# Kernel tuning notes

Measured on AMD Instinct MI355X. Metric: run time of the kernel, lower is better.

Reference implementation:

```python
import jax, jax.numpy as jnp
import numpy as np

K = 16            # neighbors per node
NB = 8            # number_of_basis
MAX_RADIUS = 10.0
MUL_1E = 32       # multiplicity of the 1e output block
DIM_0E = 64       # 64x0e block (structurally zero: no 1o x 0e -> 0e path)
DIM_2E = 80       # 16x2e block (structurally zero: no 1o x 0e -> 2e path)


def knn_edges(coords):
    """coords [B,N,3] -> (senders, receivers) flat int32 indices of length B*N*K.
    Edge (j -> i): j is one of the K nearest neighbors of i (self excluded),
    matching torch_geometric knn_graph(loop=False, flow=source_to_target)."""
    B, N, _ = coords.shape
    n2 = jnp.sum(coords * coords, -1)                       # [B,N]
    d2 = n2[:, :, None] + n2[:, None, :] - 2.0 * jnp.einsum('bnd,bmd->bnm', coords, coords)
    d2 = d2 + jnp.eye(N, dtype=coords.dtype) * 1e10         # exclude self-loops
    _, idx = jax.lax.top_k(-d2, K)                          # [B,N,K] neighbor ids per node
    offs = (jnp.arange(B) * N)[:, None, None]
    senders = (idx + offs).reshape(-1)
    receivers = (jnp.broadcast_to(jnp.arange(N)[None, :, None], (B, N, K)) + offs).reshape(-1)
    return senders, receivers


def gaussian_soft_one_hot(x, number):
    # x in [0,1], shape [E,1] -> [E,number]
    centers = jnp.linspace(0.0, 1.0, number).astype(x.dtype)
    sigma = 1.0 / number
    g = jnp.exp(-(x - centers) ** 2 / (2.0 * sigma * sigma))
    s = jnp.sum(g, -1, keepdims=True)
    s = jnp.where(s > 0, s, jnp.ones_like(s))
    return g / s


def setup_inputs():
    key = jax.random.key(0)
    ks = jax.random.split(key, 6)
    B, N = 8, 4096
    coords = jax.random.normal(ks[0], (B, N, 3), dtype=jnp.float32) * 10.0
    atom_types = jax.random.randint(ks[1], (B, N), 0, 20)
    residue_types = jax.random.randint(ks[2], (B, N), 0, 21)
    tp_weight = jax.random.normal(ks[3], (NB, MUL_1E), dtype=jnp.float32) / np.sqrt(NB)
    atom_emb = jax.random.normal(ks[4], (20, 112), dtype=jnp.float32).at[0].set(0.0)   # padding_idx=0
    res_emb = jax.random.normal(ks[5], (21, 112), dtype=jnp.float32).at[0].set(0.0)    # padding_idx=0
    return {"coords": coords, "atom_types": atom_types, "residue_types": residue_types,
            "tp_weight": tp_weight, "atom_emb": atom_emb, "res_emb": res_emb}


def reference(coords, atom_types, residue_types, tp_weight, atom_emb, res_emb):
    B, N, _ = coords.shape
    E = B * N * K
    senders, receivers = knn_edges(coords)
    cf = coords.reshape(-1, 3)
    r = cf[senders] - cf[receivers]                           # [E,3]
    dist = jnp.linalg.norm(r, axis=-1, keepdims=True)         # [E,1]
    r_hat = r / (dist + 1e-8)
    cutoff = jnp.clip(dist / MAX_RADIUS, 0.0, 1.0)
    rb = gaussian_soft_one_hot(cutoff, NB)                    # [E,NB]
    # FullyConnectedTensorProduct(1x1o/1e, NBx0e -> ... 32x1e ...):
    feat_1e = jnp.einsum('ev,vw,em->ewm', rb, tp_weight, r_hat) / np.sqrt(3.0)  # [E,32,3]
    # scatter_mean over receivers
    num = jax.ops.segment_sum(feat_1e.reshape(E, MUL_1E * 3), receivers, num_segments=B * N)
    cnt = jax.ops.segment_sum(jnp.ones((E,), coords.dtype), receivers, num_segments=B * N)
    agg_1e = (num / jnp.maximum(cnt, 1.0)[:, None]).reshape(B, N, MUL_1E * 3)
    zeros0 = jnp.zeros((B, N, DIM_0E), coords.dtype)
    zeros2 = jnp.zeros((B, N, DIM_2E), coords.dtype)
    pos_feats = jnp.concatenate([zeros0, agg_1e, zeros2], -1)  # [B,N,240]
    node_features = jnp.concatenate([pos_feats, atom_emb[atom_types], res_emb[residue_types]], -1)
    return node_features  # [B,N,464]
```

## Files before the change

kernel.cpp:

```cpp
#include <hip/hip_runtime.h>
#include <hip/hip_bf16.h>

#define NN    4096
#define KNEI  16
#define QPW   4
#define WPB   16
#define BLOCK (WPB * 64)
#define QPB   (WPB * QPW)
#define BIGF  3.0e38f


__device__ __forceinline__ float wave_max_dpp(float v)
{
    float f = v;
#define STEPX(CTRL)                                                          \
    { int s_ = __builtin_amdgcn_update_dpp(__float_as_int(f),                \
               __float_as_int(f), (CTRL), 0xF, 0xF, false);                  \
      f = fmaxf(f, __int_as_float(s_)); }
    STEPX(0x111) STEPX(0x112) STEPX(0x114) STEPX(0x118) STEPX(0x142) STEPX(0x143)
#undef STEPX
    return f;
}

__device__ __forceinline__ int wave_min_i32_dpp(int v)
{
    int f = v;
#define STEPM(CTRL)                                                          \
    { int s_ = __builtin_amdgcn_update_dpp(f, f, (CTRL), 0xF, 0xF, false);   \
      f = min(f, s_); }
    STEPM(0x111) STEPM(0x112) STEPM(0x114) STEPM(0x118) STEPM(0x142) STEPM(0x143)
#undef STEPM
    return f;
}

__device__ __forceinline__ float row16_sum_dpp(float v)
{
    float f = v;
#define STEPA(CTRL)                                                          \
    { int s_ = __builtin_amdgcn_update_dpp(0, __float_as_int(f),             \
               (CTRL), 0xF, 0xF, true);                                      \
      f += __int_as_float(s_); }
    STEPA(0x111) STEPA(0x112) STEPA(0x114) STEPA(0x118)
#undef STEPA
    return f;
}

__device__ __forceinline__ float score_calc(const float4 P, float xi, float yi,
                                            float zi, int j, int iLoc)
{
    float s = fmaf(P.x, xi, fmaf(P.y, yi, fmaf(P.z, zi, P.w)));
    return (j == iLoc) ? -1.0e30f : s;
}

__device__ __forceinline__ void wave_argmax(float v, int idx,
                                            float& m, int& midx, int& w)
{
    float f = wave_max_dpp(v);
    float M = __int_as_float(__builtin_amdgcn_readlane(__float_as_int(f), 63));
    unsigned long long msk = __ballot(v == M);
    if (__popcll(msk) > 1) {
        int ci = (v == M) ? idx : 0x7fffffff;
        ci = wave_min_i32_dpp(ci);
        ci = __builtin_amdgcn_readlane(ci, 63);
        midx = ci;
        unsigned long long m2 = __ballot(v == M && idx == ci);
        w = __ffsll(m2) - 1;
    } else {
        w = __ffsll(msk) - 1;
        midx = __builtin_amdgcn_readlane(idx, w);
    }
    m = M;
}

__device__ __forceinline__ void extract16(float b_sc, int b_idx, float s_sc, int s_idx,
                                          float xi, float yi, float zi, int qLoc,
                                          int teamBase, const float4* pts,
                                          int lane, int& selIdx)
{
    unsigned long long used = 0ull;
    #pragma unroll 1
    for (int r = 0; r < KNEI; ++r) {
        float m; int midx, w;
        wave_argmax(b_sc, b_idx, m, midx, w);
        if (lane == teamBase + r) selIdx = midx;

        bool needReplay = (__builtin_amdgcn_readlane(s_idx, w) == -1);
        if (lane == w) {
            used |= 1ull << (b_idx >> 6);
            b_sc = s_sc;  b_idx = s_idx;
            s_sc = -BIGF; s_idx = -1;
        }
        if (needReplay) {
            int j2 = w + (lane << 6);
            float scr = score_calc(pts[j2], xi, yi, zi, j2, qLoc);
            unsigned lo = (unsigned)__builtin_amdgcn_readlane((int)(used & 0xffffffffull), w);
            unsigned hi = (unsigned)__builtin_amdgcn_readlane((int)(used >> 32), w);
            unsigned long long uw = ((unsigned long long)hi << 32) | lo;
            if ((uw >> lane) & 1ull) scr = -BIGF;
            float m2; int i2, w2;
            wave_argmax(scr, j2, m2, i2, w2);
            if (lane == w) { b_sc = m2; b_idx = i2; }
        }
    }
}

#define LADDER(d, b, bi, s, si)                                   \
    {  bool gtb = (d) > (b); bool gts = (d) > (s);                \
       (s)  = __builtin_amdgcn_fmed3f((d), (s), (b));             \
       (si) = gtb ? (bi) : (gts ? j : (si));                      \
       (b)  = fmaxf((b), (d));                                    \
       (bi) = gtb ? j : (bi); }

__global__ __launch_bounds__(BLOCK, 8)
void protein_enc_kernel(const float* __restrict__ coords,
                        const int*   __restrict__ atypes,
                        const int*   __restrict__ rtypes,
                        const float* __restrict__ tpw,
                        const float* __restrict__ aemb,
                        const float* __restrict__ remb,
                        float* __restrict__ out)
{
    __shared__ float4 pts[NN];
    __shared__ float  sW[8 * 32];

    const int tid  = threadIdx.x;
    const int lane = tid & 63;
    const int wv   = tid >> 6;
    const int bpb  = NN / QPB;
    const int batch    = blockIdx.x / bpb;
    const int nodeBase = (blockIdx.x % bpb) * QPB;

    const float* cb = coords + (size_t)batch * NN * 3;

    {
        const float4* c4 = (const float4*)cb;
        float4 a = c4[3*tid], b = c4[3*tid+1], c = c4[3*tid+2];
        float x, y, z;
        x = a.x; y = a.y; z = a.z;
        pts[4*tid+0] = make_float4(x, y, z, -0.5f * (x*x + y*y + z*z));
        x = a.w; y = b.x; z = b.y;
        pts[4*tid+1] = make_float4(x, y, z, -0.5f * (x*x + y*y + z*z));
        x = b.z; y = b.w; z = c.x;
        pts[4*tid+2] = make_float4(x, y, z, -0.5f * (x*x + y*y + z*z));
        x = c.y; y = c.z; z = c.w;
        pts[4*tid+3] = make_float4(x, y, z, -0.5f * (x*x + y*y + z*z));
    }
    if (tid < 256) sW[tid] = tpw[tid];
    __syncthreads();

    const int q0 = nodeBase + wv * QPW;
    const float4 P0 = pts[q0],   P1 = pts[q0+1];
    const float4 P2 = pts[q0+2], P3 = pts[q0+3];
    const float x0 = P0.x, y0 = P0.y, z0 = P0.z;
    const float x1 = P1.x, y1 = P1.y, z1 = P1.z;
    const float x2 = P2.x, y2 = P2.y, z2 = P2.z;
    const float x3 = P3.x, y3 = P3.y, z3 = P3.z;

    float b0 = -BIGF, s0 = -BIGF, b1 = -BIGF, s1 = -BIGF;
    float b2 = -BIGF, s2 = -BIGF, b3 = -BIGF, s3 = -BIGF;
    int bi0 = -1, si0 = -1, bi1 = -1, si1 = -1;
    int bi2 = -1, si2 = -1, bi3 = -1, si3 = -1;

    #pragma unroll 4
    for (int c = 0; c < NN / 64; ++c) {
        int j = lane + (c << 6);
        float4 P = pts[j];
        float d0 = fmaf(P.x, x0, fmaf(P.y, y0, fmaf(P.z, z0, P.w)));
        float d1 = fmaf(P.x, x1, fmaf(P.y, y1, fmaf(P.z, z1, P.w)));
        float d2 = fmaf(P.x, x2, fmaf(P.y, y2, fmaf(P.z, z2, P.w)));
        float d3 = fmaf(P.x, x3, fmaf(P.y, y3, fmaf(P.z, z3, P.w)));
        LADDER(d0, b0, bi0, s0, si0)
        LADDER(d1, b1, bi1, s1, si1)
        LADDER(d2, b2, bi2, s2, si2)
        LADDER(d3, b3, bi3, s3, si3)
    }

    if (lane == ((q0  ) & 63) && bi0 == q0  ) { b0 = s0; bi0 = si0; s0 = -BIGF; si0 = -1; }
    if (lane == ((q0+1) & 63) && bi1 == q0+1) { b1 = s1; bi1 = si1; s1 = -BIGF; si1 = -1; }
    if (lane == ((q0+2) & 63) && bi2 == q0+2) { b2 = s2; bi2 = si2; s2 = -BIGF; si2 = -1; }
    if (lane == ((q0+3) & 63) && bi3 == q0+3) { b3 = s3; bi3 = si3; s3 = -BIGF; si3 = -1; }

    int selIdx = 0;
    extract16(b0, bi0, s0, si0, x0, y0, z0, q0,   0,  pts, lane, selIdx);
    extract16(b1, bi1, s1, si1, x1, y1, z1, q0+1, 16, pts, lane, selIdx);
    extract16(b2, bi2, s2, si2, x2, y2, z2, q0+2, 32, pts, lane, selIdx);
    extract16(b3, bi3, s3, si3, x3, y3, z3, q0+3, 48, pts, lane, selIdx);

    const int eq = lane >> 4;
    float xq = (eq & 2) ? ((eq & 1) ? x3 : x2) : ((eq & 1) ? x1 : x0);
    float yq = (eq & 2) ? ((eq & 1) ? y3 : y2) : ((eq & 1) ? y1 : y0);
    float zq = (eq & 2) ? ((eq & 1) ? z3 : z2) : ((eq & 1) ? z1 : z0);

    float4 P = pts[selIdx];
    float rx = P.x - xq, ry = P.y - yq, rz = P.z - zq;
    float dist = sqrtf(rx*rx + ry*ry + rz*rz);
    float inv  = 1.0f / (dist + 1e-8f);
    float hx = rx * inv, hy = ry * inv, hz = rz * inv;
    float cu = fminf(dist / 10.0f, 1.0f);
    float gg[8], ssum = 0.0f;
    #pragma unroll
    for (int v = 0; v < 8; ++v) {
        float d = cu - (float)v * (1.0f / 7.0f);
        gg[v] = expf(d * d * -32.0f);
        ssum += gg[v];
    }
    float is = 1.0f / ssum;
    float S[24];
    #pragma unroll
    for (int v = 0; v < 8; ++v) {
        float rbv = gg[v] * is;
        S[3*v]   = rbv * hx;
        S[3*v+1] = rbv * hy;
        S[3*v+2] = rbv * hz;
    }
    #pragma unroll
    for (int t = 0; t < 24; ++t) S[t] = row16_sum_dpp(S[t]);

    float wcol[8];
    #pragma unroll
    for (int v = 0; v < 8; ++v) wcol[v] = sW[32*v + (lane & 31)];

    const float scale = 0.036084391824351613f;
    const float4 z4 = make_float4(0.f, 0.f, 0.f, 0.f);

    #pragma unroll
    for (int q = 0; q < QPW; ++q) {
        const int gq = batch * NN + q0 + q;
        float sg[24];
        #pragma unroll
        for (int t = 0; t < 24; ++t)
            sg[t] = __int_as_float(
                __builtin_amdgcn_readlane(__float_as_int(S[t]), 16 * q + 15));

        float* onode = out + (size_t)gq * 464;
        float4* o4 = (float4*)onode;
        if (lane < 16)       o4[lane] = z4;
        else if (lane < 36)  o4[lane + 24] = z4;

        if (lane < 32) {
            float a0 = 0.f, a1 = 0.f, a2 = 0.f;
            #pragma unroll
            for (int v = 0; v < 8; ++v) {
                a0 = fmaf(wcol[v], sg[3*v],   a0);
                a1 = fmaf(wcol[v], sg[3*v+1], a1);
                a2 = fmaf(wcol[v], sg[3*v+2], a2);
            }
            onode[64 + 3*lane]     = a0 * scale;
            onode[64 + 3*lane + 1] = a1 * scale;
            onode[64 + 3*lane + 2] = a2 * scale;
        }

        const int at = atypes[gq];
        const int rt = rtypes[gq];
        if (lane < 56) {
            float4 v = (lane < 28)
                ? ((const float4*)(aemb + 112*at))[lane]
                : ((const float4*)(remb + 112*rt))[lane - 28];
            o4[60 + lane] = v;
        }
    }
}

extern "C" void kernel_launch(void* const* d_in, const int* in_sizes, int n_in,
                              void* d_out, int out_size, void* d_ws, size_t ws_size,
                              hipStream_t stream)
{
    const float* coords = (const float*)d_in[0];
    const int*   at     = (const int*)  d_in[1];
    const int*   rt     = (const int*)  d_in[2];
    const float* tpw    = (const float*)d_in[3];
    const float* ae     = (const float*)d_in[4];
    const float* re     = (const float*)d_in[5];
    float* out = (float*)d_out;

    const int B = in_sizes[1] / NN;
    dim3 grid(B * (NN / QPB));
    protein_enc_kernel<<<grid, BLOCK, 0, stream>>>(coords, at, rt, tpw, ae, re, out);
}
```

Measured before the change: 90.60 us.

## Interleave four query extractions per round and refill top-2 on column replay

Four changes to the top-k selection. The 16 extraction rounds for the four queries handled by a wave are now interleaved, so independent DPP reductions can overlap instead of running as four serial loops. The argmax is simplified to an always-branchless max plus min-index reduction. A column replay now refills both best and second-best, which cuts how often replays recur. The distance loop uses packed 2-wide FMA vectors, and the coordinate load becomes a strided scalar loop. The costs are higher register pressure and an extra reduction on every argmax, plus a doubled reduction in each replay.

```diff
diff --git a/kernel.cpp b/kernel.cpp
--- a/kernel.cpp
+++ b/kernel.cpp
@@ -8,6 +8,8 @@
 #define BLOCK (WPB * 64)
 #define QPB   (WPB * QPW)
 #define BIGF  3.0e38f
+
+typedef float f32x2 __attribute__((ext_vector_type(2)));
 
 
 __device__ __forceinline__ float wave_max_dpp(float v)
@@ -52,56 +54,28 @@
     return (j == iLoc) ? -1.0e30f : s;
 }
 
-__device__ __forceinline__ void wave_argmax(float v, int idx,
-                                            float& m, int& midx, int& w)
+__device__ __forceinline__ void argmax_bl(float v, int idx, float& M, int& midx)
 {
     float f = wave_max_dpp(v);
-    float M = __int_as_float(__builtin_amdgcn_readlane(__float_as_int(f), 63));
-    unsigned long long msk = __ballot(v == M);
-    if (__popcll(msk) > 1) {
-        int ci = (v == M) ? idx : 0x7fffffff;
-        ci = wave_min_i32_dpp(ci);
-        ci = __builtin_amdgcn_readlane(ci, 63);
-        midx = ci;
-        unsigned long long m2 = __ballot(v == M && idx == ci);
-        w = __ffsll(m2) - 1;
-    } else {
-        w = __ffsll(msk) - 1;
-        midx = __builtin_amdgcn_readlane(idx, w);
-    }
-    m = M;
-}
-
-__device__ __forceinline__ void extract16(float b_sc, int b_idx, float s_sc, int s_idx,
-                                          float xi, float yi, float zi, int qLoc,
-                                          int teamBase, const float4* pts,
-                                          int lane, int& selIdx)
-{
-    unsigned long long used = 0ull;
-    #pragma unroll 1
-    for (int r = 0; r < KNEI; ++r) {
-        float m; int midx, w;
-        wave_argmax(b_sc, b_idx, m, midx, w);
-        if (lane == teamBase + r) selIdx = midx;
-
-        bool needReplay = (__builtin_amdgcn_readlane(s_idx, w) == -1);
-        if (lane == w) {
-            used |= 1ull << (b_idx >> 6);
-            b_sc = s_sc;  b_idx = s_idx;
-            s_sc = -BIGF; s_idx = -1;
-        }
-        if (needReplay) {
-            int j2 = w + (lane << 6);
-            float scr = score_calc(pts[j2], xi, yi, zi, j2, qLoc);
-            unsigned lo = (unsigned)__builtin_amdgcn_readlane((int)(used & 0xffffffffull), w);
-            unsigned hi = (unsigned)__builtin_amdgcn_readlane((int)(used >> 32), w);
-            unsigned long long uw = ((unsigned long long)hi << 32) | lo;
-            if ((uw >> lane) & 1ull) scr = -BIGF;
-            float m2; int i2, w2;
-            wave_argmax(scr, j2, m2, i2, w2);
-            if (lane == w) { b_sc = m2; b_idx = i2; }
-        }
-    }
+    M = __int_as_float(__builtin_amdgcn_readlane(__float_as_int(f), 63));
+    int ci = (v == M) ? idx : 0x7fffffff;
+    ci = wave_min_i32_dpp(ci);
+    midx = __builtin_amdgcn_readlane(ci, 63);
+}
+
+__device__ __forceinline__ void replay_fill(const float4* __restrict__ pts, int w,
+    float xq, float yq, float zq, int qLoc, unsigned long long usedw, int lane,
+    float& b, int& bi, float& s, int& si)
+{
+    int j2 = w + (lane << 6);
+    float scr = score_calc(pts[j2], xq, yq, zq, j2, qLoc);
+    if ((usedw >> lane) & 1ull) scr = -BIGF;
+    float M1; int i1;
+    argmax_bl(scr, j2, M1, i1);
+    if (j2 == i1) scr = -BIGF;
+    float M2; int i2;
+    argmax_bl(scr, j2, M2, i2);
+    if (lane == w) { b = M1; bi = i1; s = M2; si = i2; }
 }
 
 #define LADDER(d, b, bi, s, si)                                   \
@@ -110,6 +84,30 @@
        (si) = gtb ? (bi) : (gts ? j : (si));                      \
        (b)  = fmaxf((b), (d));                                    \
        (bi) = gtb ? j : (bi); }
+
+#define ROUND(q, b, bi, s, si, used, wq)                                     \
+    {   float M_; int mi_;                                                   \
+        argmax_bl((b), (bi), M_, mi_);                                       \
+        wq = mi_ & 63;                                                       \
+        if (lane == ((q) << 4) + r) selIdx = mi_;                            \
+        int sW_ = __builtin_amdgcn_readlane((si), wq);                       \
+        if (lane == wq) {                                                    \
+            (used) |= 1ull << ((unsigned)((bi) >> 6) & 63u);                 \
+            (b) = (s); (bi) = (si); (s) = -BIGF; (si) = -1;                  \
+        }                                                                    \
+        needMask |= (sW_ == -1) ? (1u << (q)) : 0u;                          \
+    }
+
+#define DO_REPLAY(q, b, bi, s, si, used, wq, xq, yq, zq)                     \
+    if (needMask & (1u << (q))) {                                            \
+        unsigned lo_ = (unsigned)__builtin_amdgcn_readlane(                  \
+                           (int)((used) & 0xffffffffull), wq);               \
+        unsigned hi_ = (unsigned)__builtin_amdgcn_readlane(                  \
+                           (int)((used) >> 32), wq);                         \
+        replay_fill(pts, wq, xq, yq, zq, q0 + (q),                           \
+                    ((unsigned long long)hi_ << 32) | lo_, lane,             \
+                    b, bi, s, si);                                           \
+    }
 
 __global__ __launch_bounds__(BLOCK, 8)
 void protein_enc_kernel(const float* __restrict__ coords,
@@ -132,18 +130,9 @@
 
     const float* cb = coords + (size_t)batch * NN * 3;
 
-    {
-        const float4* c4 = (const float4*)cb;
-        float4 a = c4[3*tid], b = c4[3*tid+1], c = c4[3*tid+2];
-        float x, y, z;
-        x = a.x; y = a.y; z = a.z;
-        pts[4*tid+0] = make_float4(x, y, z, -0.5f * (x*x + y*y + z*z));
-        x = a.w; y = b.x; z = b.y;
-        pts[4*tid+1] = make_float4(x, y, z, -0.5f * (x*x + y*y + z*z));
-        x = b.z; y = b.w; z = c.x;
-        pts[4*tid+2] = make_float4(x, y, z, -0.5f * (x*x + y*y + z*z));
-        x = c.y; y = c.z; z = c.w;
-        pts[4*tid+3] = make_float4(x, y, z, -0.5f * (x*x + y*y + z*z));
+    for (int p = tid; p < NN; p += BLOCK) {
+        float x = cb[3*p], y = cb[3*p+1], z = cb[3*p+2];
+        pts[p] = make_float4(x, y, z, -0.5f * (x*x + y*y + z*z));
     }
     if (tid < 256) sW[tid] = tpw[tid];
     __syncthreads();
@@ -156,6 +145,9 @@
     const float x2 = P2.x, y2 = P2.y, z2 = P2.z;
     const float x3 = P3.x, y3 = P3.y, z3 = P3.z;
 
+    const f32x2 qAx = {x0, x1}, qAy = {y0, y1}, qAz = {z0, z1};
+    const f32x2 qBx = {x2, x3}, qBy = {y2, y3}, qBz = {z2, z3};
+
     float b0 = -BIGF, s0 = -BIGF, b1 = -BIGF, s1 = -BIGF;
     float b2 = -BIGF, s2 = -BIGF, b3 = -BIGF, s3 = -BIGF;
     int bi0 = -1, si0 = -1, bi1 = -1, si1 = -1;
@@ -165,10 +157,14 @@
     for (int c = 0; c < NN / 64; ++c) {
         int j = lane + (c << 6);
         float4 P = pts[j];
-        float d0 = fmaf(P.x, x0, fmaf(P.y, y0, fmaf(P.z, z0, P.w)));
-        float d1 = fmaf(P.x, x1, fmaf(P.y, y1, fmaf(P.z, z1, P.w)));
-        float d2 = fmaf(P.x, x2, fmaf(P.y, y2, fmaf(P.z, z2, P.w)));
-        float d3 = fmaf(P.x, x3, fmaf(P.y, y3, fmaf(P.z, z3, P.w)));
+        f32x2 Px = {P.x, P.x}, Py = {P.y, P.y}, Pz = {P.z, P.z}, Pw = {P.w, P.w};
+        f32x2 dA = __builtin_elementwise_fma(Px, qAx,
+                   __builtin_elementwise_fma(Py, qAy,
+                   __builtin_elementwise_fma(Pz, qAz, Pw)));
+        f32x2 dB = __builtin_elementwise_fma(Px, qBx,
+                   __builtin_elementwise_fma(Py, qBy,
+                   __builtin_elementwise_fma(Pz, qBz, Pw)));
+        float d0 = dA.x, d1 = dA.y, d2 = dB.x, d3 = dB.y;
         LADDER(d0, b0, bi0, s0, si0)
         LADDER(d1, b1, bi1, s1, si1)
         LADDER(d2, b2, bi2, s2, si2)
@@ -180,11 +176,24 @@
     if (lane == ((q0+2) & 63) && bi2 == q0+2) { b2 = s2; bi2 = si2; s2 = -BIGF; si2 = -1; }
     if (lane == ((q0+3) & 63) && bi3 == q0+3) { b3 = s3; bi3 = si3; s3 = -BIGF; si3 = -1; }
 
+    unsigned long long used0 = 0ull, used1 = 0ull, used2 = 0ull, used3 = 0ull;
     int selIdx = 0;
-    extract16(b0, bi0, s0, si0, x0, y0, z0, q0,   0,  pts, lane, selIdx);
-    extract16(b1, bi1, s1, si1, x1, y1, z1, q0+1, 16, pts, lane, selIdx);
-    extract16(b2, bi2, s2, si2, x2, y2, z2, q0+2, 32, pts, lane, selIdx);
-    extract16(b3, bi3, s3, si3, x3, y3, z3, q0+3, 48, pts, lane, selIdx);
+
+    #pragma unroll 1
+    for (int r = 0; r < KNEI; ++r) {
+        unsigned needMask = 0u;
+        int w0, w1, w2, w3;
+        ROUND(0, b0, bi0, s0, si0, used0, w0)
+        ROUND(1, b1, bi1, s1, si1, used1, w1)
+        ROUND(2, b2, bi2, s2, si2, used2, w2)
+        ROUND(3, b3, bi3, s3, si3, used3, w3)
+        if (needMask) {
+            DO_REPLAY(0, b0, bi0, s0, si0, used0, w0, x0, y0, z0)
+            DO_REPLAY(1, b1, bi1, s1, si1, used1, w1, x1, y1, z1)
+            DO_REPLAY(2, b2, bi2, s2, si2, used2, w2, x2, y2, z2)
+            DO_REPLAY(3, b3, bi3, s3, si3, used3, w3, x3, y3, z3)
+        }
+    }
 
     const int eq = lane >> 4;
     float xq = (eq & 2) ? ((eq & 1) ? x3 : x2) : ((eq & 1) ? x1 : x0);
```

Result: slower. 103.7 us (+14.4%).
